# Optimization experiments

Measured on AMD Instinct MI355X. Metric: run time of the kernel, lower is better.

Reference implementation:

```python
import jax, jax.numpy as jnp
import numpy as np

HEADS, HEAD_DIM = 8, 32
FOLD_W = FOLD_H = 8
PW = PH = 2  # proposal_w/h -> M = PW*PH centers per region


def setup_inputs() -> dict:
    key = jax.random.key(0)
    ks = jax.random.split(key, 8)
    dim, hd = 96, HEADS * HEAD_DIM
    return {
        "x": jax.random.normal(ks[0], (16, dim, 64, 64), jnp.float32),
        "Wf": jax.random.normal(ks[1], (hd, dim), jnp.float32) * 0.05,
        "bf": jax.random.normal(ks[2], (hd,), jnp.float32) * 0.01,
        "Wv": jax.random.normal(ks[3], (hd, dim), jnp.float32) * 0.05,
        "bv": jax.random.normal(ks[4], (hd,), jnp.float32) * 0.01,
        "Wp": jax.random.normal(ks[5], (dim, hd), jnp.float32) * 0.05,
        "bp": jax.random.normal(ks[6], (dim,), jnp.float32) * 0.01,
        "sim_alpha": jnp.ones((1,), jnp.float32),
        "sim_beta": jnp.zeros((1,), jnp.float32),
    }


def _l2norm(t):
    # matches torch F.normalize(dim=-1, eps=1e-12)
    n = jnp.maximum(jnp.linalg.norm(t, axis=-1, keepdims=True), 1e-12)
    return t / n


def _cluster_forward(x, Wf, bf, Wv, bv, Wp, bp, sim_alpha, sim_beta):
    B, C, W, H = x.shape
    # 1x1 convs
    v = jnp.einsum("bchw,oc->bohw", x, Wv) + bv[None, :, None, None]
    f = jnp.einsum("bchw,oc->bohw", x, Wf) + bf[None, :, None, None]

    def split_heads(t):  # b (e c) w h -> (b e) c w h
        b = t.shape[0]
        return t.reshape(b, HEADS, HEAD_DIM, W, H).reshape(b * HEADS, HEAD_DIM, W, H)

    f, v = split_heads(f), split_heads(v)

    def fold(t):  # b c (f1 w) (f2 h) -> (b f1 f2) c w h
        b, c, w0, h0 = t.shape
        ws, hs = w0 // FOLD_W, h0 // FOLD_H
        t = t.reshape(b, c, FOLD_W, ws, FOLD_H, hs)
        return t.transpose(0, 2, 4, 1, 3, 5).reshape(b * FOLD_W * FOLD_H, c, ws, hs)

    f, v = fold(f), fold(v)
    b, c, w, h = f.shape

    def pool(t):  # AdaptiveMaxPool2d((PW,PH)); divides evenly -> block max
        return t.reshape(b, c, PW, w // PW, PH, h // PH).max(axis=(3, 5))

    centers = pool(f).reshape(b, c, PW * PH).transpose(0, 2, 1)       # [b,M,c]
    value_centers = pool(v).reshape(b, c, PW * PH).transpose(0, 2, 1)  # [b,M,c]
    pts = f.reshape(b, c, w * h).transpose(0, 2, 1)                    # [b,N,c]

    cos = jnp.einsum("bmc,bnc->bmn", _l2norm(centers), _l2norm(pts))
    sim = jax.nn.sigmoid(sim_beta + sim_alpha * cos)                   # [b,M,N]

    # hard assignment: each point keeps only its best center
    idx = jnp.argmax(sim, axis=1)                                      # [b,N]
    mask = jax.nn.one_hot(idx, sim.shape[1], dtype=sim.dtype)          # [b,N,M]
    mask = jnp.transpose(mask, (0, 2, 1))                              # [b,M,N]
    sim = sim * mask

    value2 = v.reshape(b, c, w * h).transpose(0, 2, 1)                 # [b,N,c]
    # gather points -> centers
    agg = (jnp.einsum("bnc,bmn->bmc", value2, sim) + value_centers) / (
        mask.sum(axis=-1, keepdims=True) + 1.0
    )
    # dispatch centers -> points
    out = jnp.einsum("bmc,bmn->bnc", agg, sim)                         # [b,N,c]
    out = out.transpose(0, 2, 1).reshape(b, c, w, h)

    # unfold regions back
    bb = b // (FOLD_W * FOLD_H)
    out = out.reshape(bb, FOLD_W, FOLD_H, c, w, h).transpose(0, 3, 1, 4, 2, 5)
    out = out.reshape(bb, c, FOLD_W * w, FOLD_H * h)
    # merge heads: (b e) c w h -> b (e c) w h
    out = out.reshape(bb // HEADS, HEADS * HEAD_DIM, W, H)
    out = jnp.einsum("bchw,oc->bohw", out, Wp) + bp[None, :, None, None]
    return out


def reference(x, Wf, bf, Wv, bv, Wp, bp, sim_alpha, sim_beta):
    return _cluster_forward(x, Wf, bf, Wv, bv, Wp, bp, sim_alpha, sim_beta)
```

## Files before the change

kernel.cpp:

```cpp
#include <hip/hip_runtime.h>
#include <math.h>


#define TPB 256

__global__ __launch_bounds__(TPB, 4)
void cc_main(const float* __restrict__ x,
             const float* __restrict__ Wf, const float* __restrict__ bf,
             const float* __restrict__ Wv, const float* __restrict__ bv,
             const float* __restrict__ salpha, const float* __restrict__ sbeta,
             float* __restrict__ disp)
{
    __shared__ __align__(16) float smem[8320];
    __shared__ float cfs[2][132], cvs[2][132], swb[2][256], aggs[2][132];
    __shared__ float2 bib[2][64];
    __shared__ float cnts[2][4];

    const int t    = threadIdx.x;
    const int lane = t & 63;
    const int wid  = __builtin_amdgcn_readfirstlane(t >> 6);
    const int tc   = t >> 4;
    const int tp   = t & 15;
    const int blk  = blockIdx.x;
    const int f1   = blk & 7;
    const int f2   = (blk >> 3) & 7;
    const int heg  = (blk >> 6) & 3;
    const int bb   = blk >> 8;
    const int fold = f1*8 + f2;

    const float* xb = x + (size_t)bb*96*4096 + (size_t)(f1*8)*64 + f2*8;

    float acc[8][4];
    {
        const float* bsrc = (tc < 8) ? (bf + heg*64 + tc*8)
                                     : (bv + heg*64 + (tc-8)*8);
        float4 b0 = *(const float4*)bsrc;
        float4 b1 = *(const float4*)(bsrc + 4);
        #pragma unroll
        for (int i = 0; i < 4; ++i) {
            acc[0][i]=b0.x; acc[1][i]=b0.y; acc[2][i]=b0.z; acc[3][i]=b0.w;
            acc[4][i]=b1.x; acc[5][i]=b1.y; acc[6][i]=b1.z; acc[7][i]=b1.w;
        }
    }

    int xoff[2], xdst[2];
    #pragma unroll
    for (int i = 0; i < 2; ++i) {
        int fl = i*256 + t;
        int kl = fl >> 4, sg = fl & 15;
        xoff[i] = kl*4096 + (sg >> 1)*64 + (sg & 1)*4;
        xdst[i] = 4096 + kl*64 + sg*4;
    }
    int wdst[4];
    const float* wptr[4];
    #pragma unroll
    for (int i = 0; i < 4; ++i) {
        int fl = i*256 + t;
        int rr = fl & 127, kq = fl >> 7;
        wptr[i] = ((rr < 64) ? (Wf + (size_t)(heg*64 + rr)*96)
                             : (Wv + (size_t)(heg*64 + rr - 64)*96)) + kq*4;
        wdst[i] = (kq*4)*128 + rr;
    }

    float4 pxr[2], pwr[4];
    #pragma unroll
    for (int i = 0; i < 2; ++i) pxr[i] = *(const float4*)(xb + xoff[i]);
    #pragma unroll
    for (int i = 0; i < 4; ++i) pwr[i] = *(const float4*)(wptr[i]);
    #pragma unroll
    for (int i = 0; i < 2; ++i) *(float4*)&smem[xdst[i]] = pxr[i];
    #pragma unroll
    for (int i = 0; i < 4; ++i) {
        smem[wdst[i]      ] = pwr[i].x;
        smem[wdst[i] + 128] = pwr[i].y;
        smem[wdst[i] + 256] = pwr[i].z;
        smem[wdst[i] + 384] = pwr[i].w;
    }
    __syncthreads();

    for (int kc = 0; ; ) {
        if (kc < 64) {
            #pragma unroll
            for (int i = 0; i < 2; ++i)
                pxr[i] = *(const float4*)(xb + (kc+32)*4096 + xoff[i]);
            #pragma unroll
            for (int i = 0; i < 4; ++i)
                pwr[i] = *(const float4*)(wptr[i] + kc + 32);
        }
        #pragma unroll 4
        for (int k = 0; k < 32; ++k) {
            float4 wa  = *(const float4*)&smem[k*128 + tc*8];
            float4 wb4 = *(const float4*)&smem[k*128 + tc*8 + 4];
            float4 xq  = *(const float4*)&smem[4096 + k*64 + tp*4];
            float xv[4] = {xq.x, xq.y, xq.z, xq.w};
            #pragma unroll
            for (int i = 0; i < 4; ++i) {
                acc[0][i] = fmaf(wa.x,  xv[i], acc[0][i]);
                acc[1][i] = fmaf(wa.y,  xv[i], acc[1][i]);
                acc[2][i] = fmaf(wa.z,  xv[i], acc[2][i]);
                acc[3][i] = fmaf(wa.w,  xv[i], acc[3][i]);
                acc[4][i] = fmaf(wb4.x, xv[i], acc[4][i]);
                acc[5][i] = fmaf(wb4.y, xv[i], acc[5][i]);
                acc[6][i] = fmaf(wb4.z, xv[i], acc[6][i]);
                acc[7][i] = fmaf(wb4.w, xv[i], acc[7][i]);
            }
        }
        if (kc == 64) break;
        __syncthreads();
        #pragma unroll
        for (int i = 0; i < 2; ++i) *(float4*)&smem[xdst[i]] = pxr[i];
        #pragma unroll
        for (int i = 0; i < 4; ++i) {
            smem[wdst[i]      ] = pwr[i].x;
            smem[wdst[i] + 128] = pwr[i].y;
            smem[wdst[i] + 256] = pwr[i].z;
            smem[wdst[i] + 384] = pwr[i].w;
        }
        __syncthreads();
        kc += 32;
    }

    const float alpha = salpha[0], beta = sbeta[0];
    __syncthreads();
    #pragma unroll
    for (int j = 0; j < 8; ++j)
        #pragma unroll
        for (int i2 = 0; i2 < 4; ++i2)
            smem[(tc*8 + j)*65 + tp*4 + i2] = acc[j][i2];
    __syncthreads();

    if (wid < 2) {
        const int he = wid, slot = he;
        {
            int m = lane >> 4, c0 = (lane & 15)*2;
            int pw = m >> 1, ph = m & 1;
            #pragma unroll
            for (int cc = 0; cc < 2; ++cc) {
                int c = c0 + cc;
                float mf = -3.402823466e38f, mv = -3.402823466e38f;
                #pragma unroll
                for (int a = 0; a < 4; ++a)
                    #pragma unroll
                    for (int b2 = 0; b2 < 4; ++b2) {
                        int n = (pw*4 + a)*8 + ph*4 + b2;
                        mf = fmaxf(mf, smem[(he*32 + c)*65 + n]);
                        mv = fmaxf(mv, smem[(64 + he*32 + c)*65 + n]);
                    }
                cfs[slot][m*33 + c] = mf;
                cvs[slot][m*33 + c] = mv;
            }
        }
        float d0=0,d1=0,d2=0,d3=0,pn=0,cn0=0,cn1=0,cn2=0,cn3=0;
        #pragma unroll 8
        for (int c = 0; c < 32; ++c) {
            float fv = smem[(he*32 + c)*65 + lane];
            float m0 = cfs[slot][c], m1 = cfs[slot][33+c];
            float m2 = cfs[slot][66+c], m3 = cfs[slot][99+c];
            d0 = fmaf(m0, fv, d0); d1 = fmaf(m1, fv, d1);
            d2 = fmaf(m2, fv, d2); d3 = fmaf(m3, fv, d3);
            pn = fmaf(fv, fv, pn);
            cn0 = fmaf(m0, m0, cn0); cn1 = fmaf(m1, m1, cn1);
            cn2 = fmaf(m2, m2, cn2); cn3 = fmaf(m3, m3, cn3);
        }
        float ip = 1.f / fmaxf(sqrtf(pn), 1e-12f);
        float z0 = beta + alpha*(d0*(1.f/fmaxf(sqrtf(cn0),1e-12f))*ip);
        float z1 = beta + alpha*(d1*(1.f/fmaxf(sqrtf(cn1),1e-12f))*ip);
        float z2 = beta + alpha*(d2*(1.f/fmaxf(sqrtf(cn2),1e-12f))*ip);
        float z3 = beta + alpha*(d3*(1.f/fmaxf(sqrtf(cn3),1e-12f))*ip);
        float s0 = 1.f/(1.f + expf(-z0));
        float s1 = 1.f/(1.f + expf(-z1));
        float s2 = 1.f/(1.f + expf(-z2));
        float s3 = 1.f/(1.f + expf(-z3));
        int bi = 0; float bvv = s0;
        if (s1 > bvv) { bvv = s1; bi = 1; }
        if (s2 > bvv) { bvv = s2; bi = 2; }
        if (s3 > bvv) { bvv = s3; bi = 3; }
        int cnt0 = __popcll(__ballot(bi == 0));
        int cnt1 = __popcll(__ballot(bi == 1));
        int cnt2 = __popcll(__ballot(bi == 2));
        int cnt3 = __popcll(__ballot(bi == 3));
        swb[slot][lane]       = (bi==0) ? bvv : 0.f;
        swb[slot][64 + lane]  = (bi==1) ? bvv : 0.f;
        swb[slot][128 + lane] = (bi==2) ? bvv : 0.f;
        swb[slot][192 + lane] = (bi==3) ? bvv : 0.f;
        bib[slot][lane] = make_float2(bvv, (float)bi);
        if (lane == 0) {
            cnts[slot][0] = (float)cnt0; cnts[slot][1] = (float)cnt1;
            cnts[slot][2] = (float)cnt2; cnts[slot][3] = (float)cnt3;
        }
    }
    __syncthreads();

    if (wid >= 2) {
        const int he = wid - 2, slot = he;
        const int cI = lane & 31;
        #pragma unroll
        for (int it = 0; it < 2; ++it) {
            int mm = it*2 + (lane >> 5);
            float s = 0.f;
            #pragma unroll 8
            for (int n2 = 0; n2 < 64; ++n2)
                s = fmaf(smem[(64 + he*32 + cI)*65 + n2],
                         swb[slot][mm*64 + n2], s);
            aggs[slot][mm*33 + cI] = (s + cvs[slot][mm*33 + cI])
                                   / (cnts[slot][mm] + 1.f);
        }
        float2 b2 = bib[slot][lane];
        float bvv = b2.x; int bi = (int)b2.y;
        const int e32 = (heg*2 + he)*32;
        const size_t tbase = ((size_t)(bb*64 + fold))*16384
                           + (size_t)e32*64 + lane;
        #pragma unroll 4
        for (int c = 0; c < 32; ++c)
            disp[tbase + (size_t)c*64] = aggs[slot][bi*33 + c] * bvv;
    }
}

__global__ __launch_bounds__(192, 3)
void cc_proj(const float* __restrict__ disp, const float* __restrict__ Wp,
             const float* __restrict__ bp, float* __restrict__ out)
{
    __shared__ __align__(16) float wch[3200];
    __shared__ __align__(16) float xch[2048];
    const int t   = threadIdx.x;
    const int cg  = t >> 4;
    const int pg  = t & 15;
    const int blk = blockIdx.x;
    const int f1  = blk & 7;
    const int f2  = (blk >> 3) & 7;
    const int bb  = blk >> 6;
    const float* tb = disp + ((size_t)(bb*64 + f1*8 + f2))*16384;

    float acc[8][4];
    {
        const float* bsrc = bp + cg*8;
        float4 b0 = *(const float4*)bsrc, b1 = *(const float4*)(bsrc + 4);
        float bj[8] = {b0.x,b0.y,b0.z,b0.w,b1.x,b1.y,b1.z,b1.w};
        #pragma unroll
        for (int j = 0; j < 8; ++j)
            #pragma unroll
            for (int i = 0; i < 4; ++i) acc[j][i] = bj[j];
    }

    int wdst[4]; int woff[4];
    #pragma unroll
    for (int i = 0; i < 4; ++i) {
        int fl = i*192 + t;
        int rr = fl % 96, kq = fl / 96;
        woff[i] = rr*256 + kq*4;
        wdst[i] = (kq*4)*100 + rr;
    }
    int xoff[3];
    #pragma unroll
    for (int i = 0; i < 3; ++i) xoff[i] = (i*192 + t)*4;
    const bool x3 = (t < 128);

    float4 pwr[4], pxr[3];
    #pragma unroll
    for (int i = 0; i < 4; ++i) pwr[i] = *(const float4*)(Wp + woff[i]);
    pxr[0] = *(const float4*)(tb + xoff[0]);
    pxr[1] = *(const float4*)(tb + xoff[1]);
    if (x3) pxr[2] = *(const float4*)(tb + xoff[2]);
    #pragma unroll
    for (int i = 0; i < 4; ++i) {
        wch[wdst[i]      ] = pwr[i].x; wch[wdst[i] + 100] = pwr[i].y;
        wch[wdst[i] + 200] = pwr[i].z; wch[wdst[i] + 300] = pwr[i].w;
    }
    *(float4*)&xch[xoff[0]] = pxr[0];
    *(float4*)&xch[xoff[1]] = pxr[1];
    if (x3) *(float4*)&xch[xoff[2]] = pxr[2];
    __syncthreads();

    for (int kc = 0; ; ) {
        if (kc < 224) {
            #pragma unroll
            for (int i = 0; i < 4; ++i)
                pwr[i] = *(const float4*)(Wp + woff[i] + kc + 32);
            pxr[0] = *(const float4*)(tb + (kc+32)*64 + xoff[0]);
            pxr[1] = *(const float4*)(tb + (kc+32)*64 + xoff[1]);
            if (x3) pxr[2] = *(const float4*)(tb + (kc+32)*64 + xoff[2]);
        }
        #pragma unroll 4
        for (int k = 0; k < 32; ++k) {
            float4 wa = *(const float4*)&wch[k*100 + cg*8];
            float4 wb = *(const float4*)&wch[k*100 + cg*8 + 4];
            float4 xq = *(const float4*)&xch[k*64 + pg*4];
            float wv[8] = {wa.x,wa.y,wa.z,wa.w,wb.x,wb.y,wb.z,wb.w};
            float xv[4] = {xq.x,xq.y,xq.z,xq.w};
            #pragma unroll
            for (int j = 0; j < 8; ++j)
                #pragma unroll
                for (int i = 0; i < 4; ++i)
                    acc[j][i] = fmaf(wv[j], xv[i], acc[j][i]);
        }
        if (kc == 224) break;
        __syncthreads();
        #pragma unroll
        for (int i = 0; i < 4; ++i) {
            wch[wdst[i]      ] = pwr[i].x; wch[wdst[i] + 100] = pwr[i].y;
            wch[wdst[i] + 200] = pwr[i].z; wch[wdst[i] + 300] = pwr[i].w;
        }
        *(float4*)&xch[xoff[0]] = pxr[0];
        *(float4*)&xch[xoff[1]] = pxr[1];
        if (x3) *(float4*)&xch[xoff[2]] = pxr[2];
        __syncthreads();
        kc += 32;
    }

    const size_t ob = (size_t)bb*96*4096 + (size_t)(f1*8 + (pg >> 1))*64
                    + f2*8 + (pg & 1)*4;
    #pragma unroll
    for (int j = 0; j < 8; ++j) {
        float4 st = make_float4(acc[j][0], acc[j][1], acc[j][2], acc[j][3]);
        *(float4*)&out[ob + (size_t)(cg*8 + j)*4096] = st;
    }
}

extern "C" void kernel_launch(void* const* d_in, const int* in_sizes, int n_in,
                              void* d_out, int out_size, void* d_ws, size_t ws_size,
                              hipStream_t stream) {
    (void)in_sizes; (void)n_in; (void)out_size; (void)ws_size;
    float* disp = (float*)d_ws;
    cc_main<<<dim3(4096), dim3(TPB), 0, stream>>>(
        (const float*)d_in[0],
        (const float*)d_in[1],
        (const float*)d_in[2],
        (const float*)d_in[3],
        (const float*)d_in[4],
        (const float*)d_in[7],
        (const float*)d_in[8],
        disp);
    cc_proj<<<dim3(1024), dim3(192), 0, stream>>>(
        disp,
        (const float*)d_in[5],
        (const float*)d_in[6],
        (float*)d_out);
}
```

Before: 244.4 us.

## Project cluster centers through Wp before dispatch instead of projecting every point

Each point's output is its assigned center's aggregate scaled by its similarity, so the 256→96 projection can be applied to the four aggregated centers per region and head group before dispatch. cc_main now computes Wp·agg for each center and writes those, along with each point's (similarity, index) pair, into a compact 4096-float workspace per region. The new cc_comb kernel rebuilds each output as bias plus the sum over heads of the projected center times the similarity. This removes the large dispatched intermediate and the dense per-point projection GEMM. In exchange cc_main does a small extra matvec and adds one more block barrier.

```diff
diff --git a/kernel.cpp b/kernel.cpp
--- a/kernel.cpp
+++ b/kernel.cpp
@@ -8,8 +8,9 @@
 void cc_main(const float* __restrict__ x,
              const float* __restrict__ Wf, const float* __restrict__ bf,
              const float* __restrict__ Wv, const float* __restrict__ bv,
+             const float* __restrict__ Wp,
              const float* __restrict__ salpha, const float* __restrict__ sbeta,
-             float* __restrict__ disp)
+             float* __restrict__ cd)
 {
     __shared__ __align__(16) float smem[8320];
     __shared__ float cfs[2][132], cvs[2][132], swb[2][256], aggs[2][132];
@@ -191,6 +192,8 @@
     }
     __syncthreads();
 
+    float* tb = cd + ((size_t)(bb*64 + fold))*4096;
+
     if (wid >= 2) {
         const int he = wid - 2, slot = he;
         const int cI = lane & 31;
@@ -206,133 +209,89 @@
                                    / (cnts[slot][mm] + 1.f);
         }
         float2 b2 = bib[slot][lane];
-        float bvv = b2.x; int bi = (int)b2.y;
-        const int e32 = (heg*2 + he)*32;
-        const size_t tbase = ((size_t)(bb*64 + fold))*16384
-                           + (size_t)e32*64 + lane;
-        #pragma unroll 4
+        *(float2*)&tb[3072 + (heg*2 + he)*128 + lane*2] = b2;
+    }
+    __syncthreads();
+
+    #pragma unroll
+    for (int it = 0; it < 3; ++it) {
+        int idx = it*256 + t;
+        int he  = (idx >= 384) ? 1 : 0;
+        int rem = idx - he*384;
+        int oc  = rem >> 2, m = rem & 3;
+        const float* wp = Wp + (size_t)oc*256 + heg*64 + he*32;
+        const float* ag = aggs[he] + m*33;
+        float s = 0.f;
+        #pragma unroll
         for (int c = 0; c < 32; ++c)
-            disp[tbase + (size_t)c*64] = aggs[slot][bi*33 + c] * bvv;
+            s = fmaf(wp[c], ag[c], s);
+        tb[(heg*2 + he)*384 + oc*4 + m] = s;
     }
 }
 
-__global__ __launch_bounds__(192, 3)
-void cc_proj(const float* __restrict__ disp, const float* __restrict__ Wp,
-             const float* __restrict__ bp, float* __restrict__ out)
+__global__ __launch_bounds__(TPB, 8)
+void cc_comb(const float* __restrict__ cd, const float* __restrict__ bp,
+             float* __restrict__ out)
 {
-    __shared__ __align__(16) float wch[3200];
-    __shared__ __align__(16) float xch[2048];
-    const int t   = threadIdx.x;
-    const int cg  = t >> 4;
-    const int pg  = t & 15;
-    const int blk = blockIdx.x;
-    const int f1  = blk & 7;
-    const int f2  = (blk >> 3) & 7;
-    const int bb  = blk >> 6;
-    const float* tb = disp + ((size_t)(bb*64 + f1*8 + f2))*16384;
-
-    float acc[8][4];
-    {
-        const float* bsrc = bp + cg*8;
-        float4 b0 = *(const float4*)bsrc, b1 = *(const float4*)(bsrc + 4);
-        float bj[8] = {b0.x,b0.y,b0.z,b0.w,b1.x,b1.y,b1.z,b1.w};
-        #pragma unroll
-        for (int j = 0; j < 8; ++j)
-            #pragma unroll
-            for (int i = 0; i < 4; ++i) acc[j][i] = bj[j];
-    }
-
-    int wdst[4]; int woff[4];
+    __shared__ __align__(16) float ld[4096];
+    const int t    = threadIdx.x;
+    const int lane = t & 63;
+    const int wid  = __builtin_amdgcn_readfirstlane(t >> 6);
+    const int blk  = blockIdx.x;
+    const int f1   = blk & 7;
+    const int f2   = (blk >> 3) & 7;
+    const int bb   = blk >> 6;
+    const float* tb = cd + ((size_t)(bb*64 + f1*8 + f2))*4096;
+
     #pragma unroll
     for (int i = 0; i < 4; ++i) {
-        int fl = i*192 + t;
-        int rr = fl % 96, kq = fl / 96;
-        woff[i] = rr*256 + kq*4;
-        wdst[i] = (kq*4)*100 + rr;
-    }
-    int xoff[3];
-    #pragma unroll
-    for (int i = 0; i < 3; ++i) xoff[i] = (i*192 + t)*4;
-    const bool x3 = (t < 128);
-
-    float4 pwr[4], pxr[3];
-    #pragma unroll
-    for (int i = 0; i < 4; ++i) pwr[i] = *(const float4*)(Wp + woff[i]);
-    pxr[0] = *(const float4*)(tb + xoff[0]);
-    pxr[1] = *(const float4*)(tb + xoff[1]);
-    if (x3) pxr[2] = *(const float4*)(tb + xoff[2]);
-    #pragma unroll
-    for (int i = 0; i < 4; ++i) {
-        wch[wdst[i]      ] = pwr[i].x; wch[wdst[i] + 100] = pwr[i].y;
-        wch[wdst[i] + 200] = pwr[i].z; wch[wdst[i] + 300] = pwr[i].w;
-    }
-    *(float4*)&xch[xoff[0]] = pxr[0];
-    *(float4*)&xch[xoff[1]] = pxr[1];
-    if (x3) *(float4*)&xch[xoff[2]] = pxr[2];
-    __syncthreads();
-
-    for (int kc = 0; ; ) {
-        if (kc < 224) {
-            #pragma unroll
-            for (int i = 0; i < 4; ++i)
-                pwr[i] = *(const float4*)(Wp + woff[i] + kc + 32);
-            pxr[0] = *(const float4*)(tb + (kc+32)*64 + xoff[0]);
-            pxr[1] = *(const float4*)(tb + (kc+32)*64 + xoff[1]);
-            if (x3) pxr[2] = *(const float4*)(tb + (kc+32)*64 + xoff[2]);
-        }
-        #pragma unroll 4
-        for (int k = 0; k < 32; ++k) {
-            float4 wa = *(const float4*)&wch[k*100 + cg*8];
-            float4 wb = *(const float4*)&wch[k*100 + cg*8 + 4];
-            float4 xq = *(const float4*)&xch[k*64 + pg*4];
-            float wv[8] = {wa.x,wa.y,wa.z,wa.w,wb.x,wb.y,wb.z,wb.w};
-            float xv[4] = {xq.x,xq.y,xq.z,xq.w};
-            #pragma unroll
-            for (int j = 0; j < 8; ++j)
-                #pragma unroll
-                for (int i = 0; i < 4; ++i)
-                    acc[j][i] = fmaf(wv[j], xv[i], acc[j][i]);
-        }
-        if (kc == 224) break;
-        __syncthreads();
-        #pragma unroll
-        for (int i = 0; i < 4; ++i) {
-            wch[wdst[i]      ] = pwr[i].x; wch[wdst[i] + 100] = pwr[i].y;
-            wch[wdst[i] + 200] = pwr[i].z; wch[wdst[i] + 300] = pwr[i].w;
-        }
-        *(float4*)&xch[xoff[0]] = pxr[0];
-        *(float4*)&xch[xoff[1]] = pxr[1];
-        if (x3) *(float4*)&xch[xoff[2]] = pxr[2];
-        __syncthreads();
-        kc += 32;
-    }
-
-    const size_t ob = (size_t)bb*96*4096 + (size_t)(f1*8 + (pg >> 1))*64
-                    + f2*8 + (pg & 1)*4;
-    #pragma unroll
-    for (int j = 0; j < 8; ++j) {
-        float4 st = make_float4(acc[j][0], acc[j][1], acc[j][2], acc[j][3]);
-        *(float4*)&out[ob + (size_t)(cg*8 + j)*4096] = st;
-    }
+        float4 v = *(const float4*)(tb + (t*4 + i)*4);
+        *(float4*)&ld[(t*4 + i)*4] = v;
+    }
+    __syncthreads();
+
+    const int oc0 = wid*24;
+    float acc[24];
+    #pragma unroll
+    for (int j = 0; j < 24; j += 4) {
+        float4 b = *(const float4*)(bp + oc0 + j);
+        acc[j]=b.x; acc[j+1]=b.y; acc[j+2]=b.z; acc[j+3]=b.w;
+    }
+
+    #pragma unroll
+    for (int he = 0; he < 8; ++he) {
+        float2 sv = *(const float2*)&ld[3072 + he*128 + lane*2];
+        int bi = (int)sv.y;
+        const float* pr = &ld[he*384 + bi];
+        #pragma unroll
+        for (int j = 0; j < 24; ++j)
+            acc[j] = fmaf(pr[(oc0 + j)*4], sv.x, acc[j]);
+    }
+
+    const int r = lane >> 3, hh = lane & 7;
+    const size_t ob = (size_t)bb*96*4096 + (size_t)(f1*8 + r)*64 + f2*8 + hh;
+    #pragma unroll
+    for (int j = 0; j < 24; ++j)
+        out[ob + (size_t)(oc0 + j)*4096] = acc[j];
 }
 
 extern "C" void kernel_launch(void* const* d_in, const int* in_sizes, int n_in,
                               void* d_out, int out_size, void* d_ws, size_t ws_size,
                               hipStream_t stream) {
     (void)in_sizes; (void)n_in; (void)out_size; (void)ws_size;
-    float* disp = (float*)d_ws;
+    float* cd = (float*)d_ws;
     cc_main<<<dim3(4096), dim3(TPB), 0, stream>>>(
         (const float*)d_in[0],
         (const float*)d_in[1],
         (const float*)d_in[2],
         (const float*)d_in[3],
         (const float*)d_in[4],
+        (const float*)d_in[5],
         (const float*)d_in[7],
         (const float*)d_in[8],
-        disp);
-    cc_proj<<<dim3(1024), dim3(192), 0, stream>>>(
-        disp,
-        (const float*)d_in[5],
+        cd);
+    cc_comb<<<dim3(1024), dim3(TPB), 0, stream>>>(
+        cd,
         (const float*)d_in[6],
         (float*)d_out);
 }
```

After: 209.1 us. 1.17x faster.
